# Kernel optimization log

Measured on AMD Instinct MI355X. Metric: run time of the kernel, lower is better.

## Reference

```python
import jax, jax.numpy as jnp
import numpy as np

EPS = 1e-10
TEMP = 1.0
N_ITERS = 21  # 20 + int(1.0 / temp)


def _sinkhorn(log_alpha, temp, n_iters):
    # log_alpha: (..., n, n). Alternating row/col log-normalization in log space.
    la = log_alpha / temp
    for _ in range(n_iters):
        la = la - jax.scipy.special.logsumexp(la, axis=-2, keepdims=True)
        la = la - jax.scipy.special.logsumexp(la, axis=-1, keepdims=True)
    return jnp.exp(la)


def setup_inputs() -> dict:
    key = jax.random.key(0)
    k1, k2, k3 = jax.random.split(key, 3)
    B, N, S = 256, 1024, 16
    x = jax.random.normal(k1, (B, N), dtype=jnp.float32)
    log_alpha = jax.random.normal(k2, (N, N), dtype=jnp.float32)  # learned param (init was gumbel noise)
    u = jax.random.uniform(k3, (S, N, N), dtype=jnp.float32)  # uniform draws for Gumbel noise
    return {"x": x, "log_alpha": log_alpha, "u": u}


def reference(x, log_alpha, u):
    # Gumbel noise from uniform draws: -log(eps - log(U + eps))
    noise = -jnp.log(EPS - jnp.log(u + EPS))  # (S, N, N)
    log_alpha_noise = log_alpha[None, :, :] + noise
    soft_perms = _sinkhorn(log_alpha_noise, TEMP, N_ITERS)  # (S, N, N)
    # x: (B, N) -> (1, B, N) @ (S, N, N) -> (S, B, N)
    return jnp.einsum('bn,snm->sbm', x, soft_perms)
```

## Files before the change

kernel.cpp:

```cpp
#include <hip/hip_runtime.h>
#include <math.h>

static constexpr int S_ = 16;
static constexpr int N_ = 1024;
static constexpr int B_ = 256;
static constexpr int ITERS = 21;
#define EPSC 1e-10f

using short8 = __attribute__((ext_vector_type(8))) short;
using f32x4  = __attribute__((ext_vector_type(4))) float;

__device__ __forceinline__ float bf2f(unsigned short h) {
    union { unsigned int u; float f; } v; v.u = ((unsigned int)h) << 16; return v.f;
}
__device__ __forceinline__ unsigned short f2bf(float f) {
    union { float f; unsigned int u; } v; v.f = f;
    unsigned int r = v.u + 0x7fffu + ((v.u >> 16) & 1u);
    return (unsigned short)(r >> 16);
}
__device__ __forceinline__ unsigned int pack2(float a, float b) {
    return (unsigned int)f2bf(a) | ((unsigned int)f2bf(b) << 16);
}

__device__ __forceinline__ float la0_of(float uv, float lav) {
    float t1 = __logf(uv + EPSC);
    float t2 = EPSC - t1;
    return lav - __logf(t2);
}

#define MAP_S_SLAB(bid, s, slab) \
    const int s = ((bid) & 7) + 8 * (((bid) >> 3) & 1); \
    const int slab = (bid) >> 4;

__global__ void __launch_bounds__(256)
build_K2(const float* __restrict__ u, const float* __restrict__ la,
         unsigned short* __restrict__ Kb, float* __restrict__ partial) {
    MAP_S_SLAB(blockIdx.x, s, slab)
    const int t = threadIdx.x, wv = t >> 6, l = t & 63;
    float cs[16];
    #pragma unroll
    for (int e = 0; e < 16; ++e) cs[e] = 0.f;

    const int i0 = slab * 16 + wv * 4;
    #pragma unroll
    for (int rr = 0; rr < 4; ++rr) {
        const int i = i0 + rr;
        const float* up  = u  + ((size_t)s * N_ + i) * N_;
        const float* lap = la + (size_t)i * N_;
        float kf[16];
        #pragma unroll
        for (int h = 0; h < 2; ++h) {
            const int c = h * 512 + 8 * l;
            float4 ua = *(const float4*)(up + c);
            float4 ub = *(const float4*)(up + c + 4);
            float4 la4 = *(const float4*)(lap + c);
            float4 lb4 = *(const float4*)(lap + c + 4);
            const float uf[8] = {ua.x, ua.y, ua.z, ua.w, ub.x, ub.y, ub.z, ub.w};
            const float lf[8] = {la4.x, la4.y, la4.z, la4.w, lb4.x, lb4.y, lb4.z, lb4.w};
            unsigned int pk[4];
            #pragma unroll
            for (int e = 0; e < 4; ++e) {
                float k0 = __expf(lf[2*e])   / (EPSC - __logf(uf[2*e]   + EPSC));
                float k1 = __expf(lf[2*e+1]) / (EPSC - __logf(uf[2*e+1] + EPSC));
                unsigned short b0 = f2bf(k0), b1 = f2bf(k1);
                pk[e] = (unsigned int)b0 | ((unsigned int)b1 << 16);
                kf[h*8 + 2*e]     = bf2f(b0);
                kf[h*8 + 2*e + 1] = bf2f(b1);
            }
            *(uint4*)(Kb + ((size_t)s * N_ + i) * N_ + c) =
                make_uint4(pk[0], pk[1], pk[2], pk[3]);
        }
        #pragma unroll
        for (int e = 0; e < 16; ++e) cs[e] += kf[e];
    }

    __shared__ float lds[4][1024];
    *(float4*)&lds[wv][8*l]       = make_float4(cs[0], cs[1], cs[2], cs[3]);
    *(float4*)&lds[wv][8*l + 4]   = make_float4(cs[4], cs[5], cs[6], cs[7]);
    *(float4*)&lds[wv][512 + 8*l]     = make_float4(cs[8], cs[9], cs[10], cs[11]);
    *(float4*)&lds[wv][512 + 8*l + 4] = make_float4(cs[12], cs[13], cs[14], cs[15]);
    __syncthreads();
    const int j = t * 4;
    float4 p0 = *(const float4*)&lds[0][j];
    float4 p1 = *(const float4*)&lds[1][j];
    float4 p2 = *(const float4*)&lds[2][j];
    float4 p3 = *(const float4*)&lds[3][j];
    float4 o;
    o.x = p0.x + p1.x + p2.x + p3.x;  o.y = p0.y + p1.y + p2.y + p3.y;
    o.z = p0.z + p1.z + p2.z + p3.z;  o.w = p0.w + p1.w + p2.w + p3.w;
    *(float4*)(partial + ((size_t)s * 64 + slab) * N_ + j) = o;
}

__global__ void __launch_bounds__(256)
reduce_V(const float* __restrict__ partial, float* __restrict__ V) {
    const int s = blockIdx.x >> 2;
    const int j = (blockIdx.x & 3) * 256 + threadIdx.x;
    const float* p = partial + (size_t)s * 64 * N_ + j;
    float acc = 0.f;
    #pragma unroll
    for (int q = 0; q < 64; ++q) acc += p[(size_t)q * N_];
    V[s * N_ + j] = 1.0f / acc;
}

__global__ void __launch_bounds__(256)
sink_iter(const unsigned short* __restrict__ Kb, const float* __restrict__ V,
          float* __restrict__ U, float* __restrict__ partial) {
    MAP_S_SLAB(blockIdx.x, s, slab)
    const int t = threadIdx.x, wv = t >> 6, l = t & 63;

    float v[16];
    const float* Vp = V + s * N_;
    *(float4*)&v[0]  = *(const float4*)(Vp + 8*l);
    *(float4*)&v[4]  = *(const float4*)(Vp + 8*l + 4);
    *(float4*)&v[8]  = *(const float4*)(Vp + 512 + 8*l);
    *(float4*)&v[12] = *(const float4*)(Vp + 512 + 8*l + 4);

    float cs[16];
    #pragma unroll
    for (int e = 0; e < 16; ++e) cs[e] = 0.f;

    const int i0 = slab * 16 + wv * 4;
    const unsigned short* rowp = Kb + ((size_t)s * N_ + i0) * N_;
    #pragma unroll
    for (int rr = 0; rr < 4; ++rr, rowp += N_) {
        uint4 ka = *(const uint4*)(rowp + 8*l);
        uint4 kb = *(const uint4*)(rowp + 512 + 8*l);
        float kf[16];
        kf[0]  = bf2f((unsigned short)(ka.x & 0xffffu)); kf[1]  = bf2f((unsigned short)(ka.x >> 16));
        kf[2]  = bf2f((unsigned short)(ka.y & 0xffffu)); kf[3]  = bf2f((unsigned short)(ka.y >> 16));
        kf[4]  = bf2f((unsigned short)(ka.z & 0xffffu)); kf[5]  = bf2f((unsigned short)(ka.z >> 16));
        kf[6]  = bf2f((unsigned short)(ka.w & 0xffffu)); kf[7]  = bf2f((unsigned short)(ka.w >> 16));
        kf[8]  = bf2f((unsigned short)(kb.x & 0xffffu)); kf[9]  = bf2f((unsigned short)(kb.x >> 16));
        kf[10] = bf2f((unsigned short)(kb.y & 0xffffu)); kf[11] = bf2f((unsigned short)(kb.y >> 16));
        kf[12] = bf2f((unsigned short)(kb.z & 0xffffu)); kf[13] = bf2f((unsigned short)(kb.z >> 16));
        kf[14] = bf2f((unsigned short)(kb.w & 0xffffu)); kf[15] = bf2f((unsigned short)(kb.w >> 16));
        float dot = 0.f;
        #pragma unroll
        for (int e = 0; e < 16; ++e) dot += kf[e] * v[e];
        #pragma unroll
        for (int m = 32; m >= 1; m >>= 1) dot += __shfl_xor(dot, m);
        const float ui = 1.0f / dot;
        if (l == 0) U[s * N_ + i0 + rr] = ui;
        #pragma unroll
        for (int e = 0; e < 16; ++e) cs[e] += kf[e] * ui;
    }

    __shared__ float lds[4][1024];
    *(float4*)&lds[wv][8*l]       = make_float4(cs[0], cs[1], cs[2], cs[3]);
    *(float4*)&lds[wv][8*l + 4]   = make_float4(cs[4], cs[5], cs[6], cs[7]);
    *(float4*)&lds[wv][512 + 8*l]     = make_float4(cs[8], cs[9], cs[10], cs[11]);
    *(float4*)&lds[wv][512 + 8*l + 4] = make_float4(cs[12], cs[13], cs[14], cs[15]);
    __syncthreads();
    const int j = t * 4;
    float4 p0 = *(const float4*)&lds[0][j];
    float4 p1 = *(const float4*)&lds[1][j];
    float4 p2 = *(const float4*)&lds[2][j];
    float4 p3 = *(const float4*)&lds[3][j];
    float4 o;
    o.x = p0.x + p1.x + p2.x + p3.x;  o.y = p0.y + p1.y + p2.y + p3.y;
    o.z = p0.z + p1.z + p2.z + p3.z;  o.w = p0.w + p1.w + p2.w + p3.w;
    *(float4*)(partial + ((size_t)s * 64 + slab) * N_ + j) = o;
}

__global__ void __launch_bounds__(256)
transpose_K(const unsigned short* __restrict__ Kb, unsigned short* __restrict__ KbT) {
    const int s = blockIdx.z, k0 = blockIdx.x * 64, m0 = blockIdx.y * 64;
    __shared__ unsigned short tile[64][66];
    const int t = threadIdx.x, c4 = (t & 15) * 4, rr = t >> 4;
    const unsigned short* src = Kb + (size_t)s * N_ * N_;
    unsigned short* dst = KbT + (size_t)s * N_ * N_;
    #pragma unroll
    for (int q = 0; q < 4; ++q) {
        const int r = q * 16 + rr;
        ushort4 v = *(const ushort4*)(src + (size_t)(k0 + r) * N_ + m0 + c4);
        tile[r][c4] = v.x; tile[r][c4 + 1] = v.y; tile[r][c4 + 2] = v.z; tile[r][c4 + 3] = v.w;
    }
    __syncthreads();
    #pragma unroll
    for (int q = 0; q < 4; ++q) {
        const int rm = q * 16 + rr;
        ushort4 v;
        v.x = tile[c4][rm]; v.y = tile[c4 + 1][rm];
        v.z = tile[c4 + 2][rm]; v.w = tile[c4 + 3][rm];
        *(ushort4*)(dst + (size_t)(m0 + rm) * N_ + k0 + c4) = v;
    }
}

__global__ void __launch_bounds__(256)
mfma_out(const float* __restrict__ x, const unsigned short* __restrict__ KbT,
         const float* __restrict__ U, const float* __restrict__ V,
         float* __restrict__ out) {
    const int s  = blockIdx.z;
    const int m0 = blockIdx.x * 64;
    const int b0 = blockIdx.y * 128;
    const int t  = threadIdx.x;
    const int wid = t >> 6, l = t & 63;
    const int wr = wid >> 1, wc = wid & 1;

    __shared__ alignas(16) unsigned short lsA[128 * 64];
    __shared__ alignas(16) unsigned short lsB[64 * 64];

    f32x4 acc[4][2];
    #pragma unroll
    for (int fi = 0; fi < 4; ++fi)
        #pragma unroll
        for (int fj = 0; fj < 2; ++fj)
            acc[fi][fj] = (f32x4){0.f, 0.f, 0.f, 0.f};

    const unsigned short* Bp = KbT + ((size_t)s * N_ + m0) * N_;
    const float* Up = U + s * N_;

    float4 xa[4], xb[4];
    uint4  kv[2];
    float4 ua[2], ub[2];

    auto load_tile = [&](int k0) {
        #pragma unroll
        for (int i = 0; i < 4; ++i) {
            const int Lb  = i * 4096 + t * 16;
            const int row = Lb >> 7;
            const int kb  = Lb & 127;
            const float* xp = x + (size_t)(b0 + row) * N_ + k0 + (kb >> 1);
            xa[i] = *(const float4*)xp;
            xb[i] = *(const float4*)(xp + 4);
        }
        #pragma unroll
        for (int i = 0; i < 2; ++i) {
            const int Lb  = i * 4096 + t * 16;
            const int row = Lb >> 7;
            const int kb  = Lb & 127;
            kv[i] = *(const uint4*)((const char*)Bp + (size_t)row * 2048 + (k0 << 1) + kb);
            const int ke = k0 + (kb >> 1);
            ua[i] = *(const float4*)(Up + ke);
            ub[i] = *(const float4*)(Up + ke + 4);
        }
    };

    load_tile(0);
    for (int k0 = 0; k0 < N_; k0 += 64) {
        __syncthreads();
        #pragma unroll
        for (int i = 0; i < 4; ++i) {
            const int Lb  = i * 4096 + t * 16;
            const int row = Lb >> 7;
            const int kb  = Lb & 127;
            uint4 pk = make_uint4(pack2(xa[i].x, xa[i].y), pack2(xa[i].z, xa[i].w),
                                  pack2(xb[i].x, xb[i].y), pack2(xb[i].z, xb[i].w));
            *(uint4*)((char*)lsA + (row << 7) + (kb ^ ((row & 7) << 4))) = pk;
        }
        #pragma unroll
        for (int i = 0; i < 2; ++i) {
            const int Lb  = i * 4096 + t * 16;
            const int row = Lb >> 7;
            const int kb  = Lb & 127;
            uint4 pk;
            pk.x = pack2(bf2f((unsigned short)(kv[i].x & 0xffffu)) * ua[i].x,
                         bf2f((unsigned short)(kv[i].x >> 16))     * ua[i].y);
            pk.y = pack2(bf2f((unsigned short)(kv[i].y & 0xffffu)) * ua[i].z,
                         bf2f((unsigned short)(kv[i].y >> 16))     * ua[i].w);
            pk.z = pack2(bf2f((unsigned short)(kv[i].z & 0xffffu)) * ub[i].x,
                         bf2f((unsigned short)(kv[i].z >> 16))     * ub[i].y);
            pk.w = pack2(bf2f((unsigned short)(kv[i].w & 0xffffu)) * ub[i].z,
                         bf2f((unsigned short)(kv[i].w >> 16))     * ub[i].w);
            *(uint4*)((char*)lsB + (row << 7) + (kb ^ ((row & 7) << 4))) = pk;
        }
        __syncthreads();
        if (k0 + 64 < N_) load_tile(k0 + 64);
        #pragma unroll
        for (int ks = 0; ks < 2; ++ks) {
            const int koff = ks * 64 + ((l >> 4) << 4);
            short8 afr[4], bfr[2];
            #pragma unroll
            for (int fi = 0; fi < 4; ++fi) {
                const int r = wr * 64 + fi * 16 + (l & 15);
                afr[fi] = *(const short8*)((const char*)lsA + (r << 7) + (koff ^ ((r & 7) << 4)));
            }
            #pragma unroll
            for (int fj = 0; fj < 2; ++fj) {
                const int r = wc * 32 + fj * 16 + (l & 15);
                bfr[fj] = *(const short8*)((const char*)lsB + (r << 7) + (koff ^ ((r & 7) << 4)));
            }
            #pragma unroll
            for (int fi = 0; fi < 4; ++fi)
                #pragma unroll
                for (int fj = 0; fj < 2; ++fj)
                    acc[fi][fj] = __builtin_amdgcn_mfma_f32_16x16x32_bf16(
                        afr[fi], bfr[fj], acc[fi][fj], 0, 0, 0);
        }
    }
    #pragma unroll
    for (int fj = 0; fj < 2; ++fj) {
        const int m = m0 + wc * 32 + fj * 16 + (l & 15);
        const float vm = V[s * N_ + m];
        #pragma unroll
        for (int fi = 0; fi < 4; ++fi) {
            const int b = b0 + wr * 64 + fi * 16 + ((l >> 4) << 2);
            float* op = out + ((size_t)s * B_ + b) * N_ + m;
            #pragma unroll
            for (int e = 0; e < 4; ++e)
                op[(size_t)e * N_] = acc[fi][fj][e] * vm;
        }
    }
}

__global__ void __launch_bounds__(256)
transpose_x(const float* __restrict__ x, float* __restrict__ xT) {
    __shared__ float tile[32][33];
    const int tx = threadIdx.x, ty = threadIdx.y;
    const int gx = blockIdx.x * 32, gy = blockIdx.y * 32;
    #pragma unroll
    for (int i = 0; i < 4; ++i)
        tile[ty + i * 8][tx] = x[(gy + ty + i * 8) * N_ + gx + tx];
    __syncthreads();
    #pragma unroll
    for (int i = 0; i < 4; ++i)
        xT[(size_t)(gx + ty + i * 8) * B_ + gy + tx] = tile[tx][ty + i * 8];
}

__global__ void __launch_bounds__(256)
col_pass(const float* __restrict__ u, const float* __restrict__ la,
         const float* __restrict__ r, float* __restrict__ c) {
    const int s = blockIdx.y, t = threadIdx.x;
    const int tx = t & 15, rg = t >> 4;
    const int j = blockIdx.x * 16 + tx;
    __shared__ alignas(16) float r_lds[N_];
    ((float4*)r_lds)[t] = ((const float4*)(r + s * N_))[t];
    __syncthreads();
    const float cj = c[s * N_ + j];
    const float* up = u + (size_t)s * N_ * N_;
    const int i0 = rg * 64;
    float acc = 0.f;
    #pragma unroll 4
    for (int ii = 0; ii < 64; ++ii) {
        const int i = i0 + ii;
        acc += __expf(la0_of(up[(size_t)i * N_ + j], la[i * N_ + j]) - r_lds[i] - cj);
    }
    __shared__ float sums[16][17];
    sums[rg][tx] = acc;
    __syncthreads();
    if (t < 16) {
        float tot = 0.f;
        #pragma unroll
        for (int k = 0; k < 16; ++k) tot += sums[k][t];
        c[s * N_ + blockIdx.x * 16 + t] = cj + __logf(tot);
    }
}

__global__ void __launch_bounds__(256)
row_pass(const float* __restrict__ u, const float* __restrict__ la,
         const float* __restrict__ c, float* __restrict__ r) {
    const int s = blockIdx.y, t = threadIdx.x;
    const int w = t >> 6, l = t & 63;
    const int i = blockIdx.x * 4 + w;
    __shared__ alignas(16) float c_lds[N_];
    ((float4*)c_lds)[t] = ((const float4*)(c + s * N_))[t];
    __syncthreads();
    const float ri = r[s * N_ + i];
    const float* up = u + (size_t)s * N_ * N_ + (size_t)i * N_;
    const float* lap = la + (size_t)i * N_;
    float acc = 0.f;
    #pragma unroll
    for (int k = 0; k < 16; ++k) {
        const int jj = l + (k << 6);
        acc += __expf(la0_of(up[jj], lap[jj]) - c_lds[jj] - ri);
    }
    #pragma unroll
    for (int m = 32; m >= 1; m >>= 1) acc += __shfl_xor(acc, m);
    if (l == 0) r[s * N_ + i] = ri + __logf(acc);
}

__global__ void __launch_bounds__(256)
matmul_out(const float* __restrict__ u, const float* __restrict__ la,
           const float* __restrict__ xT, const float* __restrict__ r,
           const float* __restrict__ c, float* __restrict__ out) {
    const int s = blockIdx.z, m0 = blockIdx.x * 64, b0 = blockIdx.y * 128;
    const int t = threadIdx.x, tx = t & 7, ty = t >> 3;
    __shared__ alignas(16) float Bs[16][64];
    float acc[4][8] = {};
    const float* up = u + (size_t)s * N_ * N_;
    const float* rp = r + s * N_;
    for (int k0 = 0; k0 < N_; k0 += 16) {
        __syncthreads();
        {
            const int kk = t >> 4, f4 = t & 15;
            const int k = k0 + kk;
            const float rk = rp[k];
            const float4 uv = *(const float4*)(up + (size_t)k * N_ + m0 + f4 * 4);
            const float4 lv = *(const float4*)(la + (size_t)k * N_ + m0 + f4 * 4);
            float4 p;
            p.x = __expf(la0_of(uv.x, lv.x) - rk);
            p.y = __expf(la0_of(uv.y, lv.y) - rk);
            p.z = __expf(la0_of(uv.z, lv.z) - rk);
            p.w = __expf(la0_of(uv.w, lv.w) - rk);
            *(float4*)(&Bs[kk][f4 * 4]) = p;
        }
        __syncthreads();
        #pragma unroll
        for (int kk = 0; kk < 16; ++kk) {
            const float4 a4 = *(const float4*)(xT + (size_t)(k0 + kk) * B_ + b0 + ty * 4);
            const float4 bA = *(const float4*)(&Bs[kk][tx * 8]);
            const float4 bB = *(const float4*)(&Bs[kk][tx * 8 + 4]);
            const float av[4] = {a4.x, a4.y, a4.z, a4.w};
            const float bv[8] = {bA.x, bA.y, bA.z, bA.w, bB.x, bB.y, bB.z, bB.w};
            #pragma unroll
            for (int rr = 0; rr < 4; ++rr)
                #pragma unroll
                for (int cc = 0; cc < 8; ++cc)
                    acc[rr][cc] += av[rr] * bv[cc];
        }
    }
    float cm[8];
    #pragma unroll
    for (int cc = 0; cc < 8; ++cc) cm[cc] = __expf(-c[s * N_ + m0 + tx * 8 + cc]);
    #pragma unroll
    for (int rr = 0; rr < 4; ++rr) {
        float4 o0, o1;
        o0.x = acc[rr][0] * cm[0]; o0.y = acc[rr][1] * cm[1];
        o0.z = acc[rr][2] * cm[2]; o0.w = acc[rr][3] * cm[3];
        o1.x = acc[rr][4] * cm[4]; o1.y = acc[rr][5] * cm[5];
        o1.z = acc[rr][6] * cm[6]; o1.w = acc[rr][7] * cm[7];
        float* op = out + ((size_t)s * B_ + b0 + ty * 4 + rr) * N_ + m0 + tx * 8;
        *(float4*)op       = o0;
        *(float4*)(op + 4) = o1;
    }
}

extern "C" void kernel_launch(void* const* d_in, const int* in_sizes, int n_in,
                              void* d_out, int out_size, void* d_ws, size_t ws_size,
                              hipStream_t stream) {
    (void)in_sizes; (void)n_in; (void)out_size;
    const float* x  = (const float*)d_in[0];
    const float* la = (const float*)d_in[1];
    const float* u  = (const float*)d_in[2];
    float* out = (float*)d_out;

    const size_t KN = (size_t)S_ * N_ * N_;
    const size_t need = KN * 2 * 2
                      + (size_t)2 * S_ * N_ * 4;

    if (ws_size >= need) {
        unsigned short* Kb  = (unsigned short*)d_ws;
        unsigned short* KbT = Kb + KN;
        float* partial = (float*)KbT;
        float* U = (float*)(KbT + KN);
        float* V = U + S_ * N_;

        build_K2<<<1024, 256, 0, stream>>>(u, la, Kb, partial);

        for (int it = 0; it < ITERS; ++it) {
            reduce_V<<<64, 256, 0, stream>>>(partial, V);
            sink_iter<<<1024, 256, 0, stream>>>(Kb, V, U, partial);
        }

        transpose_K<<<dim3(16, 16, 16), 256, 0, stream>>>(Kb, KbT);

        mfma_out<<<dim3(N_ / 64, B_ / 128, S_), 256, 0, stream>>>(x, KbT, U, V, out);
    } else {
        float* r  = (float*)d_ws;
        float* c  = r + S_ * N_;
        float* xT = c + S_ * N_;
        hipMemsetAsync(d_ws, 0, 2 * S_ * N_ * sizeof(float), stream);
        transpose_x<<<dim3(N_ / 32, B_ / 32), dim3(32, 8), 0, stream>>>(x, xT);
        for (int it = 0; it < ITERS; ++it) {
            col_pass<<<dim3(N_ / 16, S_), 256, 0, stream>>>(u, la, r, c);
            row_pass<<<dim3(N_ / 4, S_),  256, 0, stream>>>(u, la, c, r);
        }
        matmul_out<<<dim3(N_ / 64, B_ / 128, S_), 256, 0, stream>>>(u, la, xT, r, c, out);
    }
}
```

Measured before the change: 272.2 us.

## Split build_K into smaller slabs, skip final colsum, widen mfma_out to 8 waves

build_K2 now handles 8 rows per block across 2048 blocks. It issues every u/la load up front, using nontemporal loads for u, and accumulates column sums directly, so reduce_V on the first iteration reads 128 slabs. The last sink_iter skips its column-sum/LDS/partial writeback because V is not recomputed afterwards. mfma_out moves to 512 threads with 8 waves of 32x32 output each, lowering per-thread registers and raising the number of waves resident for latency hiding. The cost is more blocks and a larger partial buffer for the build step.

New measurement: 385.7 us. +41.7%, slower.

```diff
diff --git a/kernel.cpp b/kernel.cpp
--- a/kernel.cpp
+++ b/kernel.cpp
@@ -28,35 +28,55 @@
     return lav - __logf(t2);
 }
 
-#define MAP_S_SLAB(bid, s, slab) \
-    const int s = ((bid) & 7) + 8 * (((bid) >> 3) & 1); \
-    const int slab = (bid) >> 4;
+__device__ __forceinline__ void unpack16(const uint4& a, const uint4& b, float* kf) {
+    kf[0]  = bf2f((unsigned short)(a.x & 0xffffu)); kf[1]  = bf2f((unsigned short)(a.x >> 16));
+    kf[2]  = bf2f((unsigned short)(a.y & 0xffffu)); kf[3]  = bf2f((unsigned short)(a.y >> 16));
+    kf[4]  = bf2f((unsigned short)(a.z & 0xffffu)); kf[5]  = bf2f((unsigned short)(a.z >> 16));
+    kf[6]  = bf2f((unsigned short)(a.w & 0xffffu)); kf[7]  = bf2f((unsigned short)(a.w >> 16));
+    kf[8]  = bf2f((unsigned short)(b.x & 0xffffu)); kf[9]  = bf2f((unsigned short)(b.x >> 16));
+    kf[10] = bf2f((unsigned short)(b.y & 0xffffu)); kf[11] = bf2f((unsigned short)(b.y >> 16));
+    kf[12] = bf2f((unsigned short)(b.z & 0xffffu)); kf[13] = bf2f((unsigned short)(b.z >> 16));
+    kf[14] = bf2f((unsigned short)(b.w & 0xffffu)); kf[15] = bf2f((unsigned short)(b.w >> 16));
+}
 
 __global__ void __launch_bounds__(256)
 build_K2(const float* __restrict__ u, const float* __restrict__ la,
          unsigned short* __restrict__ Kb, float* __restrict__ partial) {
-    MAP_S_SLAB(blockIdx.x, s, slab)
+    const int bid = blockIdx.x;
+    const int s    = (bid & 7) + 8 * ((bid >> 3) & 1);
+    const int slab = bid >> 4;
     const int t = threadIdx.x, wv = t >> 6, l = t & 63;
+    const int i0 = slab * 8 + wv * 2;
+
     float cs[16];
     #pragma unroll
     for (int e = 0; e < 16; ++e) cs[e] = 0.f;
 
-    const int i0 = slab * 16 + wv * 4;
-    #pragma unroll
-    for (int rr = 0; rr < 4; ++rr) {
+    f32x4 uu[2][4];
+    float4 ll[2][4];
+    #pragma unroll
+    for (int rr = 0; rr < 2; ++rr) {
         const int i = i0 + rr;
-        const float* up  = u  + ((size_t)s * N_ + i) * N_;
-        const float* lap = la + (size_t)i * N_;
-        float kf[16];
+        const float* up  = u  + ((size_t)s * N_ + i) * N_ + 8 * l;
+        const float* lap = la + (size_t)i * N_ + 8 * l;
+        uu[rr][0] = __builtin_nontemporal_load((const f32x4*)(up));
+        uu[rr][1] = __builtin_nontemporal_load((const f32x4*)(up + 4));
+        uu[rr][2] = __builtin_nontemporal_load((const f32x4*)(up + 512));
+        uu[rr][3] = __builtin_nontemporal_load((const f32x4*)(up + 516));
+        ll[rr][0] = *(const float4*)(lap);
+        ll[rr][1] = *(const float4*)(lap + 4);
+        ll[rr][2] = *(const float4*)(lap + 512);
+        ll[rr][3] = *(const float4*)(lap + 516);
+    }
+    #pragma unroll
+    for (int rr = 0; rr < 2; ++rr) {
+        const int i = i0 + rr;
         #pragma unroll
         for (int h = 0; h < 2; ++h) {
-            const int c = h * 512 + 8 * l;
-            float4 ua = *(const float4*)(up + c);
-            float4 ub = *(const float4*)(up + c + 4);
-            float4 la4 = *(const float4*)(lap + c);
-            float4 lb4 = *(const float4*)(lap + c + 4);
-            const float uf[8] = {ua.x, ua.y, ua.z, ua.w, ub.x, ub.y, ub.z, ub.w};
-            const float lf[8] = {la4.x, la4.y, la4.z, la4.w, lb4.x, lb4.y, lb4.z, lb4.w};
+            const float uf[8] = {uu[rr][2*h][0], uu[rr][2*h][1], uu[rr][2*h][2], uu[rr][2*h][3],
+                                 uu[rr][2*h+1][0], uu[rr][2*h+1][1], uu[rr][2*h+1][2], uu[rr][2*h+1][3]};
+            const float lf[8] = {ll[rr][2*h].x, ll[rr][2*h].y, ll[rr][2*h].z, ll[rr][2*h].w,
+                                 ll[rr][2*h+1].x, ll[rr][2*h+1].y, ll[rr][2*h+1].z, ll[rr][2*h+1].w};
             unsigned int pk[4];
             #pragma unroll
             for (int e = 0; e < 4; ++e) {
@@ -64,19 +84,84 @@
                 float k1 = __expf(lf[2*e+1]) / (EPSC - __logf(uf[2*e+1] + EPSC));
                 unsigned short b0 = f2bf(k0), b1 = f2bf(k1);
                 pk[e] = (unsigned int)b0 | ((unsigned int)b1 << 16);
-                kf[h*8 + 2*e]     = bf2f(b0);
-                kf[h*8 + 2*e + 1] = bf2f(b1);
+                cs[h*8 + 2*e]     += bf2f(b0);
+                cs[h*8 + 2*e + 1] += bf2f(b1);
             }
-            *(uint4*)(Kb + ((size_t)s * N_ + i) * N_ + c) =
+            *(uint4*)(Kb + ((size_t)s * N_ + i) * N_ + h * 512 + 8 * l) =
                 make_uint4(pk[0], pk[1], pk[2], pk[3]);
         }
-        #pragma unroll
-        for (int e = 0; e < 16; ++e) cs[e] += kf[e];
     }
 
     __shared__ float lds[4][1024];
-    *(float4*)&lds[wv][8*l]       = make_float4(cs[0], cs[1], cs[2], cs[3]);
-    *(float4*)&lds[wv][8*l + 4]   = make_float4(cs[4], cs[5], cs[6], cs[7]);
+    *(float4*)&lds[wv][8*l]           = make_float4(cs[0], cs[1], cs[2], cs[3]);
+    *(float4*)&lds[wv][8*l + 4]       = make_float4(cs[4], cs[5], cs[6], cs[7]);
+    *(float4*)&lds[wv][512 + 8*l]     = make_float4(cs[8], cs[9], cs[10], cs[11]);
+    *(float4*)&lds[wv][512 + 8*l + 4] = make_float4(cs[12], cs[13], cs[14], cs[15]);
+    __syncthreads();
+    const int j = t * 4;
+    float4 p0 = *(const float4*)&lds[0][j];
+    float4 p1 = *(const float4*)&lds[1][j];
+    float4 p2 = *(const float4*)&lds[2][j];
+    float4 p3 = *(const float4*)&lds[3][j];
+    float4 o;
+    o.x = p0.x + p1.x + p2.x + p3.x;  o.y = p0.y + p1.y + p2.y + p3.y;
+    o.z = p0.z + p1.z + p2.z + p3.z;  o.w = p0.w + p1.w + p2.w + p3.w;
+    *(float4*)(partial + ((size_t)s * 128 + slab) * N_ + j) = o;
+}
+
+__global__ void __launch_bounds__(256)
+reduce_V(const float* __restrict__ partial, float* __restrict__ V, int nslab) {
+    const int s = blockIdx.x >> 2;
+    const int j = (blockIdx.x & 3) * 256 + threadIdx.x;
+    const float* p = partial + (size_t)s * nslab * N_ + j;
+    float acc = 0.f;
+    #pragma unroll 8
+    for (int q = 0; q < nslab; ++q) acc += p[(size_t)q * N_];
+    V[s * N_ + j] = 1.0f / acc;
+}
+
+__global__ void __launch_bounds__(256)
+sink_iter(const unsigned short* __restrict__ Kb, const float* __restrict__ V,
+          float* __restrict__ U, float* __restrict__ partial, int do_colsum) {
+    const int bid = blockIdx.x;
+    const int s    = (bid & 7) + 8 * ((bid >> 3) & 1);
+    const int slab = bid >> 4;
+    const int t = threadIdx.x, wv = t >> 6, l = t & 63;
+
+    float v[16];
+    const float* Vp = V + s * N_;
+    *(float4*)&v[0]  = *(const float4*)(Vp + 8*l);
+    *(float4*)&v[4]  = *(const float4*)(Vp + 8*l + 4);
+    *(float4*)&v[8]  = *(const float4*)(Vp + 512 + 8*l);
+    *(float4*)&v[12] = *(const float4*)(Vp + 512 + 8*l + 4);
+
+    float cs[16];
+    #pragma unroll
+    for (int e = 0; e < 16; ++e) cs[e] = 0.f;
+
+    const int i0 = slab * 16 + wv * 4;
+    const unsigned short* rowp = Kb + ((size_t)s * N_ + i0) * N_;
+    #pragma unroll
+    for (int rr = 0; rr < 4; ++rr, rowp += N_) {
+        uint4 ra = *(const uint4*)(rowp + 8*l);
+        uint4 rb = *(const uint4*)(rowp + 512 + 8*l);
+        float kf[16];
+        unpack16(ra, rb, kf);
+        float dot = 0.f;
+        #pragma unroll
+        for (int e = 0; e < 16; ++e) dot += kf[e] * v[e];
+        #pragma unroll
+        for (int m = 32; m >= 1; m >>= 1) dot += __shfl_xor(dot, m);
+        const float ui = 1.0f / dot;
+        if (l == 0) U[s * N_ + i0 + rr] = ui;
+        #pragma unroll
+        for (int e = 0; e < 16; ++e) cs[e] += kf[e] * ui;
+    }
+
+    if (!do_colsum) return;
+    __shared__ float lds[4][1024];
+    *(float4*)&lds[wv][8*l]           = make_float4(cs[0], cs[1], cs[2], cs[3]);
+    *(float4*)&lds[wv][8*l + 4]       = make_float4(cs[4], cs[5], cs[6], cs[7]);
     *(float4*)&lds[wv][512 + 8*l]     = make_float4(cs[8], cs[9], cs[10], cs[11]);
     *(float4*)&lds[wv][512 + 8*l + 4] = make_float4(cs[12], cs[13], cs[14], cs[15]);
     __syncthreads();
@@ -92,77 +177,6 @@
 }
 
 __global__ void __launch_bounds__(256)
-reduce_V(const float* __restrict__ partial, float* __restrict__ V) {
-    const int s = blockIdx.x >> 2;
-    const int j = (blockIdx.x & 3) * 256 + threadIdx.x;
-    const float* p = partial + (size_t)s * 64 * N_ + j;
-    float acc = 0.f;
-    #pragma unroll
-    for (int q = 0; q < 64; ++q) acc += p[(size_t)q * N_];
-    V[s * N_ + j] = 1.0f / acc;
-}
-
-__global__ void __launch_bounds__(256)
-sink_iter(const unsigned short* __restrict__ Kb, const float* __restrict__ V,
-          float* __restrict__ U, float* __restrict__ partial) {
-    MAP_S_SLAB(blockIdx.x, s, slab)
-    const int t = threadIdx.x, wv = t >> 6, l = t & 63;
-
-    float v[16];
-    const float* Vp = V + s * N_;
-    *(float4*)&v[0]  = *(const float4*)(Vp + 8*l);
-    *(float4*)&v[4]  = *(const float4*)(Vp + 8*l + 4);
-    *(float4*)&v[8]  = *(const float4*)(Vp + 512 + 8*l);
-    *(float4*)&v[12] = *(const float4*)(Vp + 512 + 8*l + 4);
-
-    float cs[16];
-    #pragma unroll
-    for (int e = 0; e < 16; ++e) cs[e] = 0.f;
-
-    const int i0 = slab * 16 + wv * 4;
-    const unsigned short* rowp = Kb + ((size_t)s * N_ + i0) * N_;
-    #pragma unroll
-    for (int rr = 0; rr < 4; ++rr, rowp += N_) {
-        uint4 ka = *(const uint4*)(rowp + 8*l);
-        uint4 kb = *(const uint4*)(rowp + 512 + 8*l);
-        float kf[16];
-        kf[0]  = bf2f((unsigned short)(ka.x & 0xffffu)); kf[1]  = bf2f((unsigned short)(ka.x >> 16));
-        kf[2]  = bf2f((unsigned short)(ka.y & 0xffffu)); kf[3]  = bf2f((unsigned short)(ka.y >> 16));
-        kf[4]  = bf2f((unsigned short)(ka.z & 0xffffu)); kf[5]  = bf2f((unsigned short)(ka.z >> 16));
-        kf[6]  = bf2f((unsigned short)(ka.w & 0xffffu)); kf[7]  = bf2f((unsigned short)(ka.w >> 16));
-        kf[8]  = bf2f((unsigned short)(kb.x & 0xffffu)); kf[9]  = bf2f((unsigned short)(kb.x >> 16));
-        kf[10] = bf2f((unsigned short)(kb.y & 0xffffu)); kf[11] = bf2f((unsigned short)(kb.y >> 16));
-        kf[12] = bf2f((unsigned short)(kb.z & 0xffffu)); kf[13] = bf2f((unsigned short)(kb.z >> 16));
-        kf[14] = bf2f((unsigned short)(kb.w & 0xffffu)); kf[15] = bf2f((unsigned short)(kb.w >> 16));
-        float dot = 0.f;
-        #pragma unroll
-        for (int e = 0; e < 16; ++e) dot += kf[e] * v[e];
-        #pragma unroll
-        for (int m = 32; m >= 1; m >>= 1) dot += __shfl_xor(dot, m);
-        const float ui = 1.0f / dot;
-        if (l == 0) U[s * N_ + i0 + rr] = ui;
-        #pragma unroll
-        for (int e = 0; e < 16; ++e) cs[e] += kf[e] * ui;
-    }
-
-    __shared__ float lds[4][1024];
-    *(float4*)&lds[wv][8*l]       = make_float4(cs[0], cs[1], cs[2], cs[3]);
-    *(float4*)&lds[wv][8*l + 4]   = make_float4(cs[4], cs[5], cs[6], cs[7]);
-    *(float4*)&lds[wv][512 + 8*l]     = make_float4(cs[8], cs[9], cs[10], cs[11]);
-    *(float4*)&lds[wv][512 + 8*l + 4] = make_float4(cs[12], cs[13], cs[14], cs[15]);
-    __syncthreads();
-    const int j = t * 4;
-    float4 p0 = *(const float4*)&lds[0][j];
-    float4 p1 = *(const float4*)&lds[1][j];
-    float4 p2 = *(const float4*)&lds[2][j];
-    float4 p3 = *(const float4*)&lds[3][j];
-    float4 o;
-    o.x = p0.x + p1.x + p2.x + p3.x;  o.y = p0.y + p1.y + p2.y + p3.y;
-    o.z = p0.z + p1.z + p2.z + p3.z;  o.w = p0.w + p1.w + p2.w + p3.w;
-    *(float4*)(partial + ((size_t)s * 64 + slab) * N_ + j) = o;
-}
-
-__global__ void __launch_bounds__(256)
 transpose_K(const unsigned short* __restrict__ Kb, unsigned short* __restrict__ KbT) {
     const int s = blockIdx.z, k0 = blockIdx.x * 64, m0 = blockIdx.y * 64;
     __shared__ unsigned short tile[64][66];
@@ -186,7 +200,7 @@
     }
 }
 
-__global__ void __launch_bounds__(256)
+__global__ void __launch_bounds__(512)
 mfma_out(const float* __restrict__ x, const unsigned short* __restrict__ KbT,
          const float* __restrict__ U, const float* __restrict__ V,
          float* __restrict__ out) {
@@ -195,14 +209,15 @@
     const int b0 = blockIdx.y * 128;
     const int t  = threadIdx.x;
     const int wid = t >> 6, l = t & 63;
-    const int wr = wid >> 1, wc = wid & 1;
+    const int wr = wid & 3;
+    const int wc = wid >> 2;
 
     __shared__ alignas(16) unsigned short lsA[128 * 64];
     __shared__ alignas(16) unsigned short lsB[64 * 64];
 
-    f32x4 acc[4][2];
-    #pragma unroll
-    for (int fi = 0; fi < 4; ++fi)
+    f32x4 acc[2][2];
+    #pragma unroll
+    for (int fi = 0; fi < 2; ++fi)
         #pragma unroll
         for (int fj = 0; fj < 2; ++fj)
             acc[fi][fj] = (f32x4){0.f, 0.f, 0.f, 0.f};
@@ -210,29 +225,28 @@
     const unsigned short* Bp = KbT + ((size_t)s * N_ + m0) * N_;
     const float* Up = U + s * N_;
 
-    float4 xa[4], xb[4];
-    uint4  kv[2];
-    float4 ua[2], ub[2];
+    float4 xa[2], xb[2];
+    uint4  kv;
+    float4 ua, ub;
 
     auto load_tile = [&](int k0) {
         #pragma unroll
-        for (int i = 0; i < 4; ++i) {
-            const int Lb  = i * 4096 + t * 16;
+        for (int i = 0; i < 2; ++i) {
+            const int Lb  = i * 8192 + t * 16;
             const int row = Lb >> 7;
             const int kb  = Lb & 127;
             const float* xp = x + (size_t)(b0 + row) * N_ + k0 + (kb >> 1);
             xa[i] = *(const float4*)xp;
             xb[i] = *(const float4*)(xp + 4);
         }
-        #pragma unroll
-        for (int i = 0; i < 2; ++i) {
-            const int Lb  = i * 4096 + t * 16;
+        {
+            const int Lb  = t * 16;
             const int row = Lb >> 7;
             const int kb  = Lb & 127;
-            kv[i] = *(const uint4*)((const char*)Bp + (size_t)row * 2048 + (k0 << 1) + kb);
+            kv = *(const uint4*)((const char*)Bp + (size_t)row * 2048 + (k0 << 1) + kb);
             const int ke = k0 + (kb >> 1);
-            ua[i] = *(const float4*)(Up + ke);
-            ub[i] = *(const float4*)(Up + ke + 4);
+            ua = *(const float4*)(Up + ke);
+            ub = *(const float4*)(Up + ke + 4);
         }
     };
 
@@ -240,28 +254,27 @@
     for (int k0 = 0; k0 < N_; k0 += 64) {
         __syncthreads();
         #pragma unroll
-        for (int i = 0; i < 4; ++i) {
-            const int Lb  = i * 4096 + t * 16;
+        for (int i = 0; i < 2; ++i) {
+            const int Lb  = i * 8192 + t * 16;
             const int row = Lb >> 7;
             const int kb  = Lb & 127;
             uint4 pk = make_uint4(pack2(xa[i].x, xa[i].y), pack2(xa[i].z, xa[i].w),
                                   pack2(xb[i].x, xb[i].y), pack2(xb[i].z, xb[i].w));
             *(uint4*)((char*)lsA + (row << 7) + (kb ^ ((row & 7) << 4))) = pk;
         }
-        #pragma unroll
-        for (int i = 0; i < 2; ++i) {
-            const int Lb  = i * 4096 + t * 16;
+        {
+            const int Lb  = t * 16;
             const int row = Lb >> 7;
             const int kb  = Lb & 127;
             uint4 pk;
-            pk.x = pack2(bf2f((unsigned short)(kv[i].x & 0xffffu)) * ua[i].x,
-                         bf2f((unsigned short)(kv[i].x >> 16))     * ua[i].y);
-            pk.y = pack2(bf2f((unsigned short)(kv[i].y & 0xffffu)) * ua[i].z,
-                         bf2f((unsigned short)(kv[i].y >> 16))     * ua[i].w);
-            pk.z = pack2(bf2f((unsigned short)(kv[i].z & 0xffffu)) * ub[i].x,
-                         bf2f((unsigned short)(kv[i].z >> 16))     * ub[i].y);
-            pk.w = pack2(bf2f((unsigned short)(kv[i].w & 0xffffu)) * ub[i].z,
-                         bf2f((unsigned short)(kv[i].w >> 16))     * ub[i].w);
+            pk.x = pack2(bf2f((unsigned short)(kv.x & 0xffffu)) * ua.x,
+                         bf2f((unsigned short)(kv.x >> 16))     * ua.y);
+            pk.y = pack2(bf2f((unsigned short)(kv.y & 0xffffu)) * ua.z,
+                         bf2f((unsigned short)(kv.y >> 16))     * ua.w);
+            pk.z = pack2(bf2f((unsigned short)(kv.z & 0xffffu)) * ub.x,
+                         bf2f((unsigned short)(kv.z >> 16))     * ub.y);
+            pk.w = pack2(bf2f((unsigned short)(kv.w & 0xffffu)) * ub.z,
+                         bf2f((unsigned short)(kv.w >> 16))     * ub.w);
             *(uint4*)((char*)lsB + (row << 7) + (kb ^ ((row & 7) << 4))) = pk;
         }
         __syncthreads();
@@ -269,10 +282,10 @@
         #pragma unroll
         for (int ks = 0; ks < 2; ++ks) {
             const int koff = ks * 64 + ((l >> 4) << 4);
-            short8 afr[4], bfr[2];
-            #pragma unroll
-            for (int fi = 0; fi < 4; ++fi) {
-                const int r = wr * 64 + fi * 16 + (l & 15);
+            short8 afr[2], bfr[2];
+            #pragma unroll
+            for (int fi = 0; fi < 2; ++fi) {
+                const int r = wr * 32 + fi * 16 + (l & 15);
                 afr[fi] = *(const short8*)((const char*)lsA + (r << 7) + (koff ^ ((r & 7) << 4)));
             }
             #pragma unroll
@@ -281,7 +294,7 @@
                 bfr[fj] = *(const short8*)((const char*)lsB + (r << 7) + (koff ^ ((r & 7) << 4)));
             }
             #pragma unroll
-            for (int fi = 0; fi < 4; ++fi)
+            for (int fi = 0; fi < 2; ++fi)
                 #pragma unroll
                 for (int fj = 0; fj < 2; ++fj)
                     acc[fi][fj] = __builtin_amdgcn_mfma_f32_16x16x32_bf16(
@@ -293,8 +306,8 @@
         const int m = m0 + wc * 32 + fj * 16 + (l & 15);
         const float vm = V[s * N_ + m];
         #pragma unroll
-        for (int fi = 0; fi < 4; ++fi) {
-            const int b = b0 + wr * 64 + fi * 16 + ((l >> 4) << 2);
+        for (int fi = 0; fi < 2; ++fi) {
+            const int b = b0 + wr * 32 + fi * 16 + ((l >> 4) << 2);
             float* op = out + ((size_t)s * B_ + b) * N_ + m;
             #pragma unroll
             for (int e = 0; e < 4; ++e)
@@ -445,21 +458,22 @@
         float* U = (float*)(KbT + KN);
         float* V = U + S_ * N_;
 
-        build_K2<<<1024, 256, 0, stream>>>(u, la, Kb, partial);
+        build_K2<<<2048, 256, 0, stream>>>(u, la, Kb, partial);
 
         for (int it = 0; it < ITERS; ++it) {
-            reduce_V<<<64, 256, 0, stream>>>(partial, V);
-            sink_iter<<<1024, 256, 0, stream>>>(Kb, V, U, partial);
+            reduce_V<<<64, 256, 0, stream>>>(partial, V, it == 0 ? 128 : 64);
+            sink_iter<<<1024, 256, 0, stream>>>(Kb, V, U, partial,
+                                                it == ITERS - 1 ? 0 : 1);
         }
 
         transpose_K<<<dim3(16, 16, 16), 256, 0, stream>>>(Kb, KbT);
 
-        mfma_out<<<dim3(N_ / 64, B_ / 128, S_), 256, 0, stream>>>(x, KbT, U, V, out);
+        mfma_out<<<dim3(N_ / 64, B_ / 128, S_), 512, 0, stream>>>(x, KbT, U, V, out);
     } else {
         float* r  = (float*)d_ws;
         float* c  = r + S_ * N_;
         float* xT = c + S_ * N_;
-        hipMemsetAsync(d_ws, 0, 2 * S_ * N_ * sizeof(float), stream);
+        (void)hipMemsetAsync(d_ws, 0, 2 * S_ * N_ * sizeof(float), stream);
         transpose_x<<<dim3(N_ / 32, B_ / 32), dim3(32, 8), 0, stream>>>(x, xT);
         for (int it = 0; it < ITERS; ++it) {
             col_pass<<<dim3(N_ / 16, S_), 256, 0, stream>>>(u, la, r, c);
```
